# Kernel optimization log

Measured on AMD Instinct MI355X. Metric: run time of the kernel, lower is better.

## Reference

```python
import jax, jax.numpy as jnp
import numpy as np
from jax.scipy.special import logsumexp

EPS_OT = 0.05      # self.eps in AttentionOT
MAX_ITER = 100     # Sinkhorn max_iter (torch early-stops; at convergence results match)


def _l2norm(x):
    # F.normalize(x, dim=-1, p=2) with eps=1e-12
    return x / jnp.maximum(jnp.linalg.norm(x, axis=-1, keepdims=True), 1e-12)


def _sinkhorn(Cmat, mu, nu, eps):
    # Cmat: (BK, M, N), mu: (BK, M), nu: (BK, N)
    log_mu = jnp.log(mu + 1e-8)
    log_nu = jnp.log(nu + 1e-8)

    def kern(u, v):
        # log Boltzmann kernel: (-C + u_i + v_j) / eps, shape (BK, M, N)
        return (-Cmat + u[..., :, None] + v[..., None, :]) / eps

    def step(carry, _):
        u, v = carry
        u = eps * (log_mu - logsumexp(kern(u, v), axis=2)) + u
        v = eps * (log_nu - logsumexp(kern(u, v), axis=1)) + v
        return (u, v), None

    u0 = jnp.zeros_like(mu)
    v0 = jnp.zeros_like(nu)
    (u, v), _ = jax.lax.scan(jax.checkpoint(step), (u0, v0), None, length=MAX_ITER)
    return jnp.exp(kern(u, v))  # transport plan T, (BK, M, N)


def setup_inputs() -> dict:
    key = jax.random.key(0)
    Nq, M, B, K, C = 64, 16, 8, 256, 512
    ks = jax.random.split(key, 8)
    s = 1.0 / np.sqrt(C)  # torch nn.Linear default init bound
    return {
        "xq": jax.random.normal(ks[0], (Nq, M, B, C), jnp.float32),
        "xk": jax.random.normal(ks[1], (B, K, C), jnp.float32),
        "xv": jax.random.normal(ks[2], (B, K, C), jnp.float32),
        "Wq": jax.random.uniform(ks[3], (C, C), jnp.float32, -s, s),
        "Wk": jax.random.uniform(ks[4], (C, C), jnp.float32, -s, s),
        "Wv": jax.random.uniform(ks[5], (C, C), jnp.float32, -s, s),
        "Wp": jax.random.uniform(ks[6], (C, C), jnp.float32, -s, s),
        "bp": jax.random.uniform(ks[7], (C,), jnp.float32, -s, s),
    }


def reference(xq, xk, xv, Wq, Wk, Wv, Wp, bp):
    Nq, M, B, C = xq.shape
    K = xk.shape[1]
    # projections (qkv_bias=False; proj has bias). dropout probs are 0 -> identity.
    q = _l2norm(xq @ Wq.T)          # (Nq, M, B, C)
    kk = _l2norm(xk @ Wk.T)         # (B, K, C)
    v = xv @ Wv.T                   # (B, K, C)
    # torch: einsum('bkc,nmbc->bnkm') then permute(0,2,3,1) -> (B,K,M,Nq)
    sim = jnp.einsum('bkc,nmbc->bkmn', kk, q).reshape(B * K, M, Nq)
    wdist = 1.0 - sim
    mu = jnp.full((B * K, M), 1.0 / M, dtype=sim.dtype)
    nu = jnp.full((B * K, Nq), 1.0 / Nq, dtype=sim.dtype)
    T = _sinkhorn(wdist, mu, nu, EPS_OT)            # (B*K, M, Nq)
    score_map = (M * Nq * sim * T).reshape(B, K, M, Nq)
    attn = T.reshape(B, K, M, Nq).transpose(3, 0, 1, 2)  # (Nq, B, K, M)
    x = jnp.einsum('nbkm,bkc->nmbc', attn, v)            # (Nq, M, B, C)
    x = x @ Wp.T + bp
    return x, score_map
```

## Files before the change

### kernel.cpp

```cpp
#include <hip/hip_runtime.h>


typedef short   short8  __attribute__((ext_vector_type(8)));
typedef float   floatx4 __attribute__((ext_vector_type(4)));
typedef unsigned int uint2e __attribute__((ext_vector_type(2)));

static __device__ __forceinline__ float fastrcp(float x) {
    return __builtin_amdgcn_rcpf(x);
}
static __device__ __forceinline__ unsigned short f2bf(float f) {
    union { float f; unsigned u; } c; c.f = f;
    unsigned r = c.u + 0x7FFF + ((c.u >> 16) & 1);
    return (unsigned short)(r >> 16);
}
static __device__ __forceinline__ float bf2f(unsigned short h) {
    union { unsigned u; float f; } c; c.u = (unsigned)h << 16;
    return c.f;
}

static __device__ __forceinline__ void gll16(const unsigned short* g, short* l) {
    __builtin_amdgcn_global_load_lds(
        (const __attribute__((address_space(1))) void*)g,
        (__attribute__((address_space(3))) void*)l, 16, 0, 0);
}

#if __has_builtin(__builtin_amdgcn_permlane16_swap)
static __device__ __forceinline__ float xadd16(float s) {
    uint2e r = __builtin_amdgcn_permlane16_swap(
        __float_as_uint(s), __float_as_uint(s), false, false);
    return __uint_as_float(r.x) + __uint_as_float(r.y);
}
#else
static __device__ __forceinline__ float xadd16(float s) {
    return s + __shfl_xor(s, 16, 64);
}
#endif
#if __has_builtin(__builtin_amdgcn_permlane32_swap)
static __device__ __forceinline__ float xadd32(float s) {
    uint2e r = __builtin_amdgcn_permlane32_swap(
        __float_as_uint(s), __float_as_uint(s), false, false);
    return __uint_as_float(r.x) + __uint_as_float(r.y);
}
#else
static __device__ __forceinline__ float xadd32(float s) {
    return s + __shfl_xor(s, 32, 64);
}
#endif

#define RRI(x, C) __builtin_amdgcn_update_dpp(0, (x), (C), 0xf, 0xf, true)
#define RRF(x, C) __int_as_float(RRI(__float_as_int(x), (C)))
#define GATH16(d, s) do { d[0] = (s);                                        \
    d[1]  = RRF((s), 0x121); d[2]  = RRF((s), 0x122);                        \
    d[3]  = RRF((s), 0x123); d[4]  = RRF((s), 0x124);                        \
    d[5]  = RRF((s), 0x125); d[6]  = RRF((s), 0x126);                        \
    d[7]  = RRF((s), 0x127); d[8]  = RRF((s), 0x128);                        \
    d[9]  = RRF((s), 0x129); d[10] = RRF((s), 0x12a);                        \
    d[11] = RRF((s), 0x12b); d[12] = RRF((s), 0x12c);                        \
    d[13] = RRF((s), 0x12d); d[14] = RRF((s), 0x12e);                        \
    d[15] = RRF((s), 0x12f); } while (0)

__global__ __launch_bounds__(256) void prep(
    const float* __restrict__ xq, const float* __restrict__ xk,
    const float* __restrict__ xv, const float* __restrict__ Wq,
    const float* __restrict__ Wk, const float* __restrict__ Wv,
    const float* __restrict__ Wp,
    unsigned short* __restrict__ xqh, unsigned short* __restrict__ xql,
    unsigned short* __restrict__ xkh, unsigned short* __restrict__ xkl,
    unsigned short* __restrict__ xvb,
    unsigned short* __restrict__ wqh, unsigned short* __restrict__ wql,
    unsigned short* __restrict__ wkh, unsigned short* __restrict__ wkl,
    unsigned short* __restrict__ wvb, unsigned short* __restrict__ wpb)
{
    const int b = blockIdx.x;
    const float* src; unsigned short *dh, *dl; long base;
    if (b < 4096)      { src = xq; dh = xqh; dl = xql;     base = (long)b * 256; }
    else if (b < 5120) { src = xk; dh = xkh; dl = xkl;     base = (long)(b - 4096) * 256; }
    else if (b < 6144) { src = xv; dh = xvb; dl = nullptr; base = (long)(b - 5120) * 256; }
    else if (b < 6400) { src = Wq; dh = wqh; dl = wql;     base = (long)(b - 6144) * 256; }
    else if (b < 6656) { src = Wk; dh = wkh; dl = wkl;     base = (long)(b - 6400) * 256; }
    else if (b < 6912) { src = Wv; dh = wvb; dl = nullptr; base = (long)(b - 6656) * 256; }
    else               { src = Wp; dh = wpb; dl = nullptr; base = (long)(b - 6912) * 256; }
    const long i = base + threadIdx.x;
    float4 v = ((const float4*)src)[i];
    ushort4 h;
    h.x = f2bf(v.x); h.y = f2bf(v.y); h.z = f2bf(v.z); h.w = f2bf(v.w);
    ((ushort4*)dh)[i] = h;
    if (dl) {
        ushort4 l;
        l.x = f2bf(v.x - bf2f(h.x)); l.y = f2bf(v.y - bf2f(h.y));
        l.z = f2bf(v.z - bf2f(h.z)); l.w = f2bf(v.w - bf2f(h.w));
        ((ushort4*)dl)[i] = l;
    }
}

__global__ __launch_bounds__(256, 3) void gemm_qkv2(
    const unsigned short* __restrict__ xqh, const unsigned short* __restrict__ xql,
    const unsigned short* __restrict__ xkh, const unsigned short* __restrict__ xkl,
    const unsigned short* __restrict__ xvb,
    const unsigned short* __restrict__ wqh, const unsigned short* __restrict__ wql,
    const unsigned short* __restrict__ wkh, const unsigned short* __restrict__ wkl,
    const unsigned short* __restrict__ wvb,
    unsigned short* __restrict__ qh, unsigned short* __restrict__ ql,
    unsigned short* __restrict__ kh, unsigned short* __restrict__ kl,
    unsigned short* __restrict__ vt)
{
    __shared__ __align__(16) short LB[24576];

    const int bt = blockIdx.x;
    const unsigned short *Ah, *Al, *Bh, *Bl;
    int seg, arow0;
    if (bt < 128)      { Ah = xqh; Al = xql; Bh = wqh; Bl = wql; arow0 = bt * 64;         seg = 0; }
    else if (bt < 160) { Ah = xkh; Al = xkl; Bh = wkh; Bl = wkl; arow0 = (bt - 128) * 64; seg = 1; }
    else               { Ah = xvb; Al = xvb; Bh = wvb; Bl = wvb; arow0 = (bt - 160) * 64; seg = 2; }
    const bool split = (seg != 2);

    const int tid  = threadIdx.x;
    const int lane = tid & 63, wv = tid >> 6;
    const int wc = wv * 32;
    const int j0 = blockIdx.y * 128;

    floatx4 acc[4][2];
#pragma unroll
    for (int i = 0; i < 4; i++)
#pragma unroll
        for (int j = 0; j < 2; j++) acc[i][j] = {0.f, 0.f, 0.f, 0.f};

    const int lrow = lane >> 2;
    const int lch  = (lane & 3) * 8;
    const int gra  = 16 * wv;
    const int grb  = 32 * wv;
    const long gA0 = (long)(arow0 + gra + lrow) * 512 + lch;
    const long gB0 = (long)(j0    + grb + lrow) * 512 + lch;

    const int fr = lane & 15, fq = (lane >> 4) * 8;

#define QKV_STAGE(d, k0) do {                                                 \
        short* bb = LB + (d) * 12288;                                         \
        gll16(Ah + gA0 + (k0),            bb + gra * 32);                     \
        gll16(Bh + gB0 + (k0),            bb + 4096 + grb * 32);              \
        gll16(Bh + gB0 + (k0) + 16 * 512, bb + 4096 + (grb + 16) * 32);       \
        if (split) {                                                          \
            gll16(Al + gA0 + (k0),            bb + 2048 + gra * 32);          \
            gll16(Bl + gB0 + (k0),            bb + 8192 + grb * 32);          \
            gll16(Bl + gB0 + (k0) + 16 * 512, bb + 8192 + (grb + 16) * 32);   \
        }                                                                     \
    } while (0)

    QKV_STAGE(0, 0);
    __syncthreads();

#pragma unroll 2
    for (int t = 0; t < 16; t++) {
        const int cur = t & 1;
        if (t < 15) QKV_STAGE(cur ^ 1, (t + 1) * 32);
        const short* base = LB + cur * 12288;
        short8 ah[4], bh[2];
#pragma unroll
        for (int i = 0; i < 4; i++)
            ah[i] = *(const short8*)&base[(i * 16 + fr) * 32 + fq];
#pragma unroll
        for (int j = 0; j < 2; j++)
            bh[j] = *(const short8*)&base[4096 + (wc + j * 16 + fr) * 32 + fq];
        if (split) {
            short8 al[4], bl[2];
#pragma unroll
            for (int i = 0; i < 4; i++)
                al[i] = *(const short8*)&base[2048 + (i * 16 + fr) * 32 + fq];
#pragma unroll
            for (int j = 0; j < 2; j++)
                bl[j] = *(const short8*)&base[8192 + (wc + j * 16 + fr) * 32 + fq];
#pragma unroll
            for (int i = 0; i < 4; i++)
#pragma unroll
                for (int j = 0; j < 2; j++) {
                    acc[i][j] = __builtin_amdgcn_mfma_f32_16x16x32_bf16(ah[i], bh[j], acc[i][j], 0, 0, 0);
                    acc[i][j] = __builtin_amdgcn_mfma_f32_16x16x32_bf16(ah[i], bl[j], acc[i][j], 0, 0, 0);
                    acc[i][j] = __builtin_amdgcn_mfma_f32_16x16x32_bf16(al[i], bh[j], acc[i][j], 0, 0, 0);
                }
        } else {
#pragma unroll
            for (int i = 0; i < 4; i++)
#pragma unroll
                for (int j = 0; j < 2; j++)
                    acc[i][j] = __builtin_amdgcn_mfma_f32_16x16x32_bf16(ah[i], bh[j], acc[i][j], 0, 0, 0);
        }
        __syncthreads();
    }
#undef QKV_STAGE

    const int cr = (lane >> 4) * 4, cc = lane & 15;
    if (seg == 2) {
        short (*S2)[72] = (short(*)[72])LB;
#pragma unroll
        for (int i = 0; i < 4; i++)
#pragma unroll
            for (int j = 0; j < 2; j++)
#pragma unroll
                for (int r = 0; r < 4; r++)
                    S2[wc + j * 16 + cc][i * 16 + cr + r] =
                        (short)f2bf(acc[i][j][r]);
        __syncthreads();
        const int orow = tid >> 1;
        const int os   = (tid & 1) * 32;
        unsigned short* dst = vt + (long)(arow0 >> 8) * 131072
                            + (long)(j0 + orow) * 256 + (arow0 & 255) + os;
#pragma unroll
        for (int c8 = 0; c8 < 4; c8++)
            *(short8*)(dst + c8 * 8) = *(const short8*)&S2[orow][os + c8 * 8];
    } else {
#pragma unroll
        for (int i = 0; i < 4; i++)
#pragma unroll
            for (int j = 0; j < 2; j++) {
                const int gj = j0 + wc + j * 16 + cc;
#pragma unroll
                for (int r = 0; r < 4; r++) {
                    const int gi = arow0 + i * 16 + cr + r;
                    const float v = acc[i][j][r];
                    const unsigned short h = f2bf(v);
                    const unsigned short lo = f2bf(v - bf2f(h));
                    if (seg == 0) {
                        const long orow = (long)((gi & 7) * 1024 + ((gi >> 3) & 15) * 64 + (gi >> 7));
                        qh[orow * 512 + gj] = h;
                        ql[orow * 512 + gj] = lo;
                    } else {
                        kh[(long)gi * 512 + gj] = h;
                        kl[(long)gi * 512 + gj] = lo;
                    }
                }
            }
    }
}

__global__ __launch_bounds__(256) void gemm_sim64(
    const short* __restrict__ Ah, const short* __restrict__ Al,
    const short* __restrict__ Bh, const short* __restrict__ Bl,
    float* __restrict__ Out)
{
    const int z = blockIdx.z;
    Ah += (long)z * 131072;  Al += (long)z * 131072;
    Bh += (long)z * 524288;  Bl += (long)z * 524288;
    Out += (long)z * 262144;

    __shared__ __align__(16) short Ash[64][40];
    __shared__ __align__(16) short Asl[64][40];
    __shared__ __align__(16) short Bsh[64][40];
    __shared__ __align__(16) short Bsl[64][40];
    __shared__ float sRA[64];
    __shared__ float sRB[64];

    const int tid  = threadIdx.x;
    const int lane = tid & 63, wv = tid >> 6;
    const int wr = (wv >> 1) * 32, wc = (wv & 1) * 32;
    const int i0 = blockIdx.x * 64, j0 = blockIdx.y * 64;

    floatx4 acc[2][2];
#pragma unroll
    for (int i = 0; i < 2; i++)
#pragma unroll
        for (int j = 0; j < 2; j++) acc[i][j] = {0.f, 0.f, 0.f, 0.f};

    const int sr = tid >> 2, sch = (tid & 3) * 8;
    const int fr = lane & 15, fq = (lane >> 4) * 8;

    float ssqA = 0.0f, ssqB = 0.0f;

    for (int k0 = 0; k0 < 512; k0 += 32) {
        const long ao = (long)(i0 + sr) * 512 + k0 + sch;
        const long bo = (long)(j0 + sr) * 512 + k0 + sch;
        const short8 vah = *(const short8*)(Ah + ao);
        const short8 val_ = *(const short8*)(Al + ao);
        const short8 vbh = *(const short8*)(Bh + bo);
        const short8 vbl = *(const short8*)(Bl + bo);
        *(short8*)&Ash[sr][sch] = vah;
        *(short8*)&Asl[sr][sch] = val_;
        *(short8*)&Bsh[sr][sch] = vbh;
        *(short8*)&Bsl[sr][sch] = vbl;
#pragma unroll
        for (int e = 0; e < 8; e++) {
            const float va = bf2f((unsigned short)vah[e]) + bf2f((unsigned short)val_[e]);
            const float vb = bf2f((unsigned short)vbh[e]) + bf2f((unsigned short)vbl[e]);
            ssqA = fmaf(va, va, ssqA);
            ssqB = fmaf(vb, vb, ssqB);
        }
        __syncthreads();
        short8 ah[2], al[2], bh[2], bl[2];
#pragma unroll
        for (int i = 0; i < 2; i++) {
            ah[i] = *(const short8*)&Ash[wr + i * 16 + fr][fq];
            al[i] = *(const short8*)&Asl[wr + i * 16 + fr][fq];
        }
#pragma unroll
        for (int j = 0; j < 2; j++) {
            bh[j] = *(const short8*)&Bsh[wc + j * 16 + fr][fq];
            bl[j] = *(const short8*)&Bsl[wc + j * 16 + fr][fq];
        }
#pragma unroll
        for (int i = 0; i < 2; i++)
#pragma unroll
            for (int j = 0; j < 2; j++) {
                acc[i][j] = __builtin_amdgcn_mfma_f32_16x16x32_bf16(ah[i], bh[j], acc[i][j], 0, 0, 0);
                acc[i][j] = __builtin_amdgcn_mfma_f32_16x16x32_bf16(ah[i], bl[j], acc[i][j], 0, 0, 0);
                acc[i][j] = __builtin_amdgcn_mfma_f32_16x16x32_bf16(al[i], bh[j], acc[i][j], 0, 0, 0);
            }
        __syncthreads();
    }

    ssqA += __shfl_xor(ssqA, 1, 64);  ssqA += __shfl_xor(ssqA, 2, 64);
    ssqB += __shfl_xor(ssqB, 1, 64);  ssqB += __shfl_xor(ssqB, 2, 64);
    if ((tid & 3) == 0) {
        sRA[sr] = 1.0f / fmaxf(sqrtf(ssqA), 1e-12f);
        sRB[sr] = 1.0f / fmaxf(sqrtf(ssqB), 1e-12f);
    }
    __syncthreads();

    const int cr = (lane >> 4) * 4, cc = lane & 15;
#pragma unroll
    for (int i = 0; i < 2; i++)
#pragma unroll
        for (int j = 0; j < 2; j++) {
            const int lc = wc + j * 16 + cc;
            const float sq = sRB[lc];
            const int gj = j0 + lc;
#pragma unroll
            for (int r = 0; r < 4; r++) {
                const int lr = wr + i * 16 + cr + r;
                Out[(long)(i0 + lr) * 1024 + gj] = acc[i][j][r] * sRA[lr] * sq;
            }
        }
}

template <bool BIAS, bool OPERM, bool OUT_BF16>
__global__ __launch_bounds__(256) void gemm_bf16(
    const short* __restrict__ A, const short* __restrict__ B,
    const float* __restrict__ bias, void* __restrict__ OutV,
    int Kdim, int lda, int ldb, int ldo, long sA, long sB, long sO)
{
    __shared__ __align__(16) short As[128][40];
    __shared__ __align__(16) short Bs[128][40];

    const int tid  = threadIdx.x;
    const int lane = tid & 63, wv = tid >> 6;
    const int wr = (wv >> 1) * 64, wc = (wv & 1) * 64;
    const int i0 = blockIdx.x * 128, j0 = blockIdx.y * 128;

    floatx4 acc[4][4];
#pragma unroll
    for (int i = 0; i < 4; i++)
#pragma unroll
        for (int j = 0; j < 4; j++) acc[i][j] = {0.f, 0.f, 0.f, 0.f};

    const int sr = tid >> 2, sk = (tid & 3) * 8;
    const int fr = lane & 15, fq = (lane >> 4) * 8;
    const short* pa = A + (long)blockIdx.z * sA;
    const short* pb = B + (long)blockIdx.z * sB;

    for (int k0 = 0; k0 < Kdim; k0 += 32) {
#pragma unroll
        for (int p = 0; p < 2; p++) {
            *(short8*)&As[sr + p * 64][sk] =
                *(const short8*)(pa + (long)(i0 + sr + p * 64) * lda + k0 + sk);
            *(short8*)&Bs[sr + p * 64][sk] =
                *(const short8*)(pb + (long)(j0 + sr + p * 64) * ldb + k0 + sk);
        }
        __syncthreads();
        short8 af[4], bf[4];
#pragma unroll
        for (int i = 0; i < 4; i++) af[i] = *(const short8*)&As[wr + i * 16 + fr][fq];
#pragma unroll
        for (int j = 0; j < 4; j++) bf[j] = *(const short8*)&Bs[wc + j * 16 + fr][fq];
#pragma unroll
        for (int i = 0; i < 4; i++)
#pragma unroll
            for (int j = 0; j < 4; j++)
                acc[i][j] = __builtin_amdgcn_mfma_f32_16x16x32_bf16(af[i], bf[j], acc[i][j], 0, 0, 0);
        __syncthreads();
    }

    float* Of = nullptr; unsigned short* Ob = nullptr;
    if constexpr (OUT_BF16) Ob = (unsigned short*)OutV + (long)blockIdx.z * sO;
    else                    Of = (float*)OutV + (long)blockIdx.z * sO;
    const int cr = (lane >> 4) * 4, cc = lane & 15;
#pragma unroll
    for (int i = 0; i < 4; i++) {
#pragma unroll
        for (int j = 0; j < 4; j++) {
            const int gj = j0 + wc + j * 16 + cc;
            float bb = 0.0f;
            if constexpr (BIAS) bb = bias[gj];
#pragma unroll
            for (int r = 0; r < 4; r++) {
                const int gi = i0 + wr + i * 16 + cr + r;
                float v = acc[i][j][r] + bb;
                long idx;
                if constexpr (OPERM)
                    idx = (long)((gi & 63) * 128 + ((gi >> 6) & 15) * 8 + (gi >> 10)) * ldo + gj;
                else
                    idx = (long)gi * ldo + gj;
                if constexpr (OUT_BF16) Ob[idx] = f2bf(v);
                else                    Of[idx] = v;
            }
        }
    }
}

__global__ __launch_bounds__(256, 2) void sinkhorn5(
    const float* __restrict__ sim, float* __restrict__ score,
    unsigned short* __restrict__ Tt)
{
    const int lane = threadIdx.x & 63;
    const int bk   = blockIdx.x * 4 + (threadIdx.x >> 6);
    const float* S = sim + (long)bk * 1024;
    const int m = lane & 15, g = lane >> 4;

    int idx[16];
    idx[0] = m;
    idx[1]  = RRI(m, 0x121); idx[2]  = RRI(m, 0x122); idx[3]  = RRI(m, 0x123);
    idx[4]  = RRI(m, 0x124); idx[5]  = RRI(m, 0x125); idx[6]  = RRI(m, 0x126);
    idx[7]  = RRI(m, 0x127); idx[8]  = RRI(m, 0x128); idx[9]  = RRI(m, 0x129);
    idx[10] = RRI(m, 0x12a); idx[11] = RRI(m, 0x12b); idx[12] = RRI(m, 0x12c);
    idx[13] = RRI(m, 0x12d); idx[14] = RRI(m, 0x12e); idx[15] = RRI(m, 0x12f);

    float K1[16], K2R[16], sv[16];
#pragma unroll
    for (int j = 0; j < 16; j++) {
        K1[j] = __expf((S[m * 64 + g * 16 + idx[j]] - 1.0f) * 20.0f);
        const float s_ = S[idx[j] * 64 + lane];
        sv[j]  = s_;
        K2R[j] = __expf((s_ - 1.0f) * 20.0f);
    }

    const float muP = 0.0625f + 1e-8f;
    const float nuP = 0.015625f + 1e-8f;
    float b = 1.0f;
    float aB[16], bB[16];
#pragma unroll
    for (int j = 0; j < 16; j++) bB[j] = 1.0f;

#pragma unroll 1
    for (int it = 0; it < 100; it++) {
        float s0 = 0, s1 = 0, s2 = 0, s3 = 0;
#pragma unroll
        for (int j = 0; j < 4; j++) {
            s0 = fmaf(K1[j],      bB[j],      s0);
            s1 = fmaf(K1[4 + j],  bB[4 + j],  s1);
            s2 = fmaf(K1[8 + j],  bB[8 + j],  s2);
            s3 = fmaf(K1[12 + j], bB[12 + j], s3);
        }
        float s = (s0 + s1) + (s2 + s3);
        s = xadd16(s);
        s = xadd32(s);
        const float a = muP * fastrcp(s);
        GATH16(aB, a);
        float t0 = 0, t1 = 0, t2 = 0, t3 = 0;
#pragma unroll
        for (int j = 0; j < 4; j++) {
            t0 = fmaf(K2R[j],      aB[j],      t0);
            t1 = fmaf(K2R[4 + j],  aB[4 + j],  t1);
            t2 = fmaf(K2R[8 + j],  aB[8 + j],  t2);
            t3 = fmaf(K2R[12 + j], aB[12 + j], t3);
        }
        const float bp_ = b;
        b = nuP * fastrcp((t0 + t1) + (t2 + t3));
        GATH16(bB, b);
        const int conv = __builtin_fabsf(b - bp_) <= 1e-5f * __builtin_fabsf(b);
        if (__all(conv)) break;
    }

    float* Sc = score + (long)bk * 1024;
    unsigned short* Tp = Tt + (long)(bk >> 8) * 262144 + (bk & 255);
#pragma unroll
    for (int j = 0; j < 16; j++) {
        const int row = idx[j];
        const float Tv = aB[j] * K2R[j] * b;
        Sc[row * 64 + lane] = 1024.0f * sv[j] * Tv;
        Tp[(long)(row * 64 + lane) * 256] = f2bf(Tv);
    }
}

extern "C" void kernel_launch(void* const* d_in, const int* in_sizes, int n_in,
                              void* d_out, int out_size, void* d_ws, size_t ws_size,
                              hipStream_t stream)
{
    (void)in_sizes; (void)n_in; (void)out_size; (void)ws_size;
    const float* xq = (const float*)d_in[0];
    const float* xk = (const float*)d_in[1];
    const float* xv = (const float*)d_in[2];
    const float* Wq = (const float*)d_in[3];
    const float* Wk = (const float*)d_in[4];
    const float* Wv = (const float*)d_in[5];
    const float* Wp = (const float*)d_in[6];
    const float* bp = (const float*)d_in[7];

    float* out_x     = (float*)d_out;
    float* out_score = out_x + 8192L * 512;

    char* W = (char*)d_ws;
    const long MB = 1 << 20;
    unsigned short* qh   = (unsigned short*)(W + 0);
    unsigned short* ql   = (unsigned short*)(W + 8 * MB);
    unsigned short* xq_h = (unsigned short*)(W + 16 * MB);
    float*          simb = (float*)(W + 16 * MB);
    unsigned short* xq_l = (unsigned short*)(W + 24 * MB);
    unsigned short* xpre = (unsigned short*)(W + 24 * MB);
    unsigned short* xk_h = (unsigned short*)(W + 32 * MB);
    unsigned short* xk_l = (unsigned short*)(W + 34 * MB);
    unsigned short* Tt   = (unsigned short*)(W + 32 * MB);
    unsigned short* xv_b = (unsigned short*)(W + 36 * MB);
    unsigned short* kh   = (unsigned short*)(W + 38 * MB);
    unsigned short* kl   = (unsigned short*)(W + 40 * MB);
    unsigned short* vt   = (unsigned short*)(W + 42 * MB);
    unsigned short* wqh  = (unsigned short*)(W + 44 * MB);
    unsigned short* wql  = (unsigned short*)(W + 44 * MB + 1 * 524288);
    unsigned short* wkh  = (unsigned short*)(W + 44 * MB + 2 * 524288);
    unsigned short* wkl  = (unsigned short*)(W + 44 * MB + 3 * 524288);
    unsigned short* wvb  = (unsigned short*)(W + 44 * MB + 4 * 524288);
    unsigned short* wpb  = (unsigned short*)(W + 44 * MB + 5 * 524288);

    const dim3 blk(256);

    prep<<<7168, blk, 0, stream>>>(xq, xk, xv, Wq, Wk, Wv, Wp,
                                   xq_h, xq_l, xk_h, xk_l, xv_b,
                                   wqh, wql, wkh, wkl, wvb, wpb);

    gemm_qkv2<<<dim3(192, 4), blk, 0, stream>>>(
        xq_h, xq_l, xk_h, xk_l, xv_b, wqh, wql, wkh, wkl, wvb,
        qh, ql, kh, kl, vt);

    gemm_sim64<<<dim3(4, 16, 8), blk, 0, stream>>>(
        (const short*)kh, (const short*)kl, (const short*)qh, (const short*)ql,
        simb);

    sinkhorn5<<<512, blk, 0, stream>>>(simb, out_score, Tt);

    gemm_bf16<false, false, true><<<dim3(8, 4, 8), blk, 0, stream>>>(
        (const short*)Tt, (const short*)vt, nullptr, xpre,
        256, 256, 256, 512, 262144, 131072, 524288);

    gemm_bf16<true, true, false><<<dim3(64, 4), blk, 0, stream>>>(
        (const short*)xpre, (const short*)wpb, bp, out_x,
        512, 512, 512, 512, 0, 0, 0);
}
```

Measured before the change: 186.8 us.

## Double-buffer bf16 GEMM with direct global-to-LDS loads and smaller tiles

Replaces the register-staged bf16 GEMM with a version that loads tiles straight into LDS using global_load_lds. The loads are double-buffered so the next K-slice is fetched while MFMAs run on the current one. The block tile shrinks from 128x128 to 64x128 with 4 waves splitting N, which doubles the grid for the two small final GEMMs to improve occupancy. The unpadded LDS layout may cause bank conflicts, and the smaller tiles reduce reuse per block.

```diff
diff --git a/kernel.cpp b/kernel.cpp
--- a/kernel.cpp
+++ b/kernel.cpp
@@ -331,51 +331,67 @@
 }
 
 template <bool BIAS, bool OPERM, bool OUT_BF16>
-__global__ __launch_bounds__(256) void gemm_bf16(
-    const short* __restrict__ A, const short* __restrict__ B,
+__global__ __launch_bounds__(256, 2) void gemm_bf16_v2(
+    const unsigned short* __restrict__ A, const unsigned short* __restrict__ B,
     const float* __restrict__ bias, void* __restrict__ OutV,
     int Kdim, int lda, int ldb, int ldo, long sA, long sB, long sO)
 {
-    __shared__ __align__(16) short As[128][40];
-    __shared__ __align__(16) short Bs[128][40];
+    __shared__ __align__(16) short LB[12288];
 
     const int tid  = threadIdx.x;
     const int lane = tid & 63, wv = tid >> 6;
-    const int wr = (wv >> 1) * 64, wc = (wv & 1) * 64;
-    const int i0 = blockIdx.x * 128, j0 = blockIdx.y * 128;
-
-    floatx4 acc[4][4];
+    const int wc = wv * 32;
+    const int i0 = blockIdx.x * 64, j0 = blockIdx.y * 128;
+
+    floatx4 acc[4][2];
 #pragma unroll
     for (int i = 0; i < 4; i++)
 #pragma unroll
-        for (int j = 0; j < 4; j++) acc[i][j] = {0.f, 0.f, 0.f, 0.f};
-
-    const int sr = tid >> 2, sk = (tid & 3) * 8;
+        for (int j = 0; j < 2; j++) acc[i][j] = {0.f, 0.f, 0.f, 0.f};
+
+    const unsigned short* pa = A + (long)blockIdx.z * sA;
+    const unsigned short* pb = B + (long)blockIdx.z * sB;
+
+    const int lrow = lane >> 2;
+    const int lch  = (lane & 3) * 8;
+    const int gra  = 16 * wv;
+    const int grb  = 32 * wv;
+    const long gA0 = (long)(i0 + gra + lrow) * lda + lch;
+    const long gB0 = (long)(j0 + grb + lrow) * ldb + lch;
+
     const int fr = lane & 15, fq = (lane >> 4) * 8;
-    const short* pa = A + (long)blockIdx.z * sA;
-    const short* pb = B + (long)blockIdx.z * sB;
-
-    for (int k0 = 0; k0 < Kdim; k0 += 32) {
-#pragma unroll
-        for (int p = 0; p < 2; p++) {
-            *(short8*)&As[sr + p * 64][sk] =
-                *(const short8*)(pa + (long)(i0 + sr + p * 64) * lda + k0 + sk);
-            *(short8*)&Bs[sr + p * 64][sk] =
-                *(const short8*)(pb + (long)(j0 + sr + p * 64) * ldb + k0 + sk);
-        }
-        __syncthreads();
-        short8 af[4], bf[4];
-#pragma unroll
-        for (int i = 0; i < 4; i++) af[i] = *(const short8*)&As[wr + i * 16 + fr][fq];
-#pragma unroll
-        for (int j = 0; j < 4; j++) bf[j] = *(const short8*)&Bs[wc + j * 16 + fr][fq];
+
+#define BF2_STAGE(d, k0) do {                                                 \
+        short* bb = LB + (d) * 6144;                                          \
+        gll16(pa + gA0 + (k0),             bb + gra * 32);                    \
+        gll16(pb + gB0 + (k0),             bb + 2048 + grb * 32);             \
+        gll16(pb + gB0 + (k0) + 16 * ldb,  bb + 2048 + (grb + 16) * 32);      \
+    } while (0)
+
+    const int nt = Kdim >> 5;
+    BF2_STAGE(0, 0);
+    __syncthreads();
+
+#pragma unroll 2
+    for (int t = 0; t < nt; t++) {
+        const int cur = t & 1;
+        if (t < nt - 1) BF2_STAGE(cur ^ 1, (t + 1) * 32);
+        const short* base = LB + cur * 6144;
+        short8 af[4], bf[2];
 #pragma unroll
         for (int i = 0; i < 4; i++)
-#pragma unroll
-            for (int j = 0; j < 4; j++)
+            af[i] = *(const short8*)&base[(i * 16 + fr) * 32 + fq];
+#pragma unroll
+        for (int j = 0; j < 2; j++)
+            bf[j] = *(const short8*)&base[2048 + (wc + j * 16 + fr) * 32 + fq];
+#pragma unroll
+        for (int i = 0; i < 4; i++)
+#pragma unroll
+            for (int j = 0; j < 2; j++)
                 acc[i][j] = __builtin_amdgcn_mfma_f32_16x16x32_bf16(af[i], bf[j], acc[i][j], 0, 0, 0);
         __syncthreads();
     }
+#undef BF2_STAGE
 
     float* Of = nullptr; unsigned short* Ob = nullptr;
     if constexpr (OUT_BF16) Ob = (unsigned short*)OutV + (long)blockIdx.z * sO;
@@ -384,13 +400,13 @@
 #pragma unroll
     for (int i = 0; i < 4; i++) {
 #pragma unroll
-        for (int j = 0; j < 4; j++) {
+        for (int j = 0; j < 2; j++) {
             const int gj = j0 + wc + j * 16 + cc;
             float bb = 0.0f;
             if constexpr (BIAS) bb = bias[gj];
 #pragma unroll
             for (int r = 0; r < 4; r++) {
-                const int gi = i0 + wr + i * 16 + cr + r;
+                const int gi = i0 + i * 16 + cr + r;
                 float v = acc[i][j][r] + bb;
                 long idx;
                 if constexpr (OPERM)
@@ -533,11 +549,11 @@
 
     sinkhorn5<<<512, blk, 0, stream>>>(simb, out_score, Tt);
 
-    gemm_bf16<false, false, true><<<dim3(8, 4, 8), blk, 0, stream>>>(
-        (const short*)Tt, (const short*)vt, nullptr, xpre,
+    gemm_bf16_v2<false, false, true><<<dim3(16, 4, 8), blk, 0, stream>>>(
+        Tt, vt, nullptr, xpre,
         256, 256, 256, 512, 262144, 131072, 524288);
 
-    gemm_bf16<true, true, false><<<dim3(64, 4), blk, 0, stream>>>(
-        (const short*)xpre, (const short*)wpb, bp, out_x,
+    gemm_bf16_v2<true, true, false><<<dim3(128, 4), blk, 0, stream>>>(
+        xpre, wpb, bp, out_x,
         512, 512, 512, 512, 0, 0, 0);
 }
```

Result: faster. 180.4 us (-3.4%).
